# Kernel tuning notes

Measured on AMD Instinct MI355X. Metric: run time of the kernel, lower is better.

## Reference

```python
import jax, jax.numpy as jnp
import numpy as np

H = 512        # rnn_h
E = 256        # embedding_dim
ATD = 32       # action_type_emb_dim
VOCAB = 50000  # data_agent.wordcnt
NUM_ACTIONS = 10
CHECK_WEIGHT = 1.0
B, SIN, SOUT, Y = 32, 128, 32, 256
DIN = 2 * H + 1 + E + ATD + E  # dec_gru input size (y_in=True, bidir=True)


def gru_step(h, x, Wih, Whh, bih, bhh):
    # PyTorch GRUCell math
    gi = x @ Wih.T + bih
    gh = h @ Whh.T + bhh
    ir, iz, i_n = jnp.split(gi, 3, axis=-1)
    hr, hz, h_n = jnp.split(gh, 3, axis=-1)
    r = jax.nn.sigmoid(ir + hr)
    z = jax.nn.sigmoid(iz + hz)
    n = jnp.tanh(i_n + r * h_n)
    return (1.0 - z) * n + z * h


def setup_inputs() -> dict:
    key = jax.random.key(0)
    ks = iter(jax.random.split(key, 48))

    def p(shape, scale=0.05):
        return jax.random.normal(next(ks), shape, dtype=jnp.float32) * scale

    inp = {}
    inp["x"] = jax.random.randint(next(ks), (B, SIN), 0, VOCAB)
    inp["action_key"] = jax.random.randint(next(ks), (Y,), 0, VOCAB)
    inp["action_type"] = jax.random.randint(next(ks), (Y,), 0, NUM_ACTIONS + 1)
    inp["current_room"] = jax.random.randint(next(ks), (B, SOUT), 0, VOCAB)
    inp["checked"] = jax.random.uniform(next(ks), (B, SOUT + 1, Y), dtype=jnp.float32)
    inp["y"] = jax.random.uniform(next(ks), (B, SOUT, Y), dtype=jnp.float32)
    emb = p((VOCAB, E))
    inp["emb_table"] = emb.at[0].set(0.0)  # padding_idx=0
    inp["atype_table"] = p((NUM_ACTIONS + 1, ATD))
    # encoder GRU, bidirectional, 1 layer
    inp["enc_Wih_f"] = p((3 * H, E)); inp["enc_Whh_f"] = p((3 * H, H))
    inp["enc_bih_f"] = p((3 * H,));   inp["enc_bhh_f"] = p((3 * H,))
    inp["enc_Wih_b"] = p((3 * H, E)); inp["enc_Whh_b"] = p((3 * H, H))
    inp["enc_bih_b"] = p((3 * H,));   inp["enc_bhh_b"] = p((3 * H,))
    inp["trans_W"] = p((E, 2 * H)); inp["trans_b"] = p((E,))
    inp["merge_W"] = p((H, 2 * H)); inp["merge_b"] = p((H,))
    inp["dec_Wih"] = p((3 * H, DIN)); inp["dec_Whh"] = p((3 * H, H))
    inp["dec_bih"] = p((3 * H,));     inp["dec_bhh"] = p((3 * H,))
    inp["dec_W"] = p((1, H)); inp["dec_b"] = p((1,))
    inp["chk_W1"] = p((H, 2 * H + ATD + H)); inp["chk_b1"] = p((H,))
    inp["chk_W2"] = p((1, H));               inp["chk_b2"] = p((1,))
    return inp


def reference(x, action_key, action_type, current_room, checked, y,
              emb_table, atype_table,
              enc_Wih_f, enc_Whh_f, enc_bih_f, enc_bhh_f,
              enc_Wih_b, enc_Whh_b, enc_bih_b, enc_bhh_b,
              trans_W, trans_b, merge_W, merge_b,
              dec_Wih, dec_Whh, dec_bih, dec_bhh, dec_W, dec_b,
              chk_W1, chk_b1, chk_W2, chk_b2):
    emb_out = emb_table[x]  # [B, SIN, E]

    def enc_scan(Wih, Whh, bih, bhh, xs):  # xs: [S, B, E]
        def step(h, xt):
            h2 = gru_step(h, xt, Wih, Whh, bih, bhh)
            return h2, h2
        h0 = jnp.zeros((B, H), emb_out.dtype)
        return jax.lax.scan(step, h0, xs)

    xs = emb_out.transpose(1, 0, 2)
    hT_f, hs_f = enc_scan(enc_Wih_f, enc_Whh_f, enc_bih_f, enc_bhh_f, xs)
    hT_b, hs_b = enc_scan(enc_Wih_b, enc_Whh_b, enc_bih_b, enc_bhh_b, xs[::-1])
    hs_b = hs_b[::-1]
    enc_out = jnp.concatenate([hs_f, hs_b], axis=-1).transpose(1, 0, 2)  # [B, SIN, 2H]

    action_emb = emb_table[action_key]  # [Y, E]
    trans_out = jnp.tanh(enc_out @ trans_W.T + trans_b)  # [B, SIN, E]
    scores = (jnp.einsum('bse,ye->bys', emb_out, action_emb)
              + jnp.einsum('bse,ye->bys', trans_out, action_emb))
    alpha = jax.nn.softmax(scores, axis=-1)
    attention = jnp.einsum('bys,bsd->byd', alpha, enc_out)  # [B, Y, 2H]

    atype_exp = jnp.broadcast_to(atype_table[action_type], (B, Y, ATD))
    room_emb = emb_table[current_room]  # [B, SOUT, E]

    # faithful to torch: hidden [2,B,H].view(B, 2H) (layer-major flatten)
    hidden_cat = jnp.stack([hT_f, hT_b], 0).reshape(B, 2 * H)
    h0_dec = jnp.tanh(hidden_cat @ merge_W.T + merge_b)  # [B, H]
    h_dec = jnp.broadcast_to(h0_dec[:, None, :], (B, Y, H)).reshape(B * Y, H)

    y_prev = jnp.concatenate([jnp.zeros((B, 1, Y), y.dtype), y[:, :-1]], axis=1)

    att_flat = attention.reshape(B * Y, 2 * H)
    at_flat = atype_exp.reshape(B * Y, ATD)

    xs_scan = (checked[:, :SOUT].transpose(1, 0, 2),   # check_in  [T,B,Y]
               room_emb.transpose(1, 0, 2),            # room      [T,B,E]
               y_prev.transpose(1, 0, 2),              # y_{t-1}   [T,B,Y]
               y.transpose(1, 0, 2),                   # y_t       [T,B,Y]
               checked[:, 1:].transpose(1, 0, 2))      # check tgt [T,B,Y]

    def step(h, inputs):
        chk_t, room_t, yp_t, y_t, chk_next = inputs
        room_in = jnp.broadcast_to(room_t[:, None, :], (B, Y, E))
        y_in = jnp.broadcast_to((yp_t @ action_emb)[:, None, :], (B, Y, E))
        dec_in = jnp.concatenate(
            [attention, chk_t[..., None], room_in, atype_exp, y_in], axis=-1
        ).reshape(B * Y, DIN)
        h2 = gru_step(h, dec_in, dec_Wih, dec_Whh, dec_bih, dec_bhh)
        logits = (h2 @ dec_W.T + dec_b).reshape(B, Y)
        logp = jax.nn.log_softmax(logits, axis=1)
        l = -(logp * y_t).sum()
        cat = jnp.concatenate([att_flat, at_flat, h2], axis=1)
        chk = jax.nn.sigmoid(jnp.tanh(cat @ chk_W1.T + chk_b1) @ chk_W2.T + chk_b2).reshape(B, Y)
        cl = -((chk_next * jnp.log(chk) + (1.0 - chk_next) * jnp.log(1.0 - chk)) * y_t).sum() * CHECK_WEIGHT
        return h2, (l, cl)

    _, (ls, cls) = jax.lax.scan(step, h_dec, xs_scan)
    ysum = y.sum()
    loss = ls.sum() / ysum
    check_loss = cls.sum() / ysum
    return (loss + check_loss, loss, check_loss)
```

## Files before the change

kernel.cpp:

```cpp
#include <hip/hip_runtime.h>

typedef unsigned short ushort;
typedef unsigned int uint;
typedef __attribute__((ext_vector_type(8))) short short8;
typedef __attribute__((ext_vector_type(4))) float f32x4;
typedef __attribute__((ext_vector_type(4))) uint u32x4;

#define DEVI __device__ __forceinline__

#define B_ 32
#define SIN_ 128
#define SOUT_ 32
#define Y_ 256
#define H_ 512
#define E_ 256
#define TH_ 1536

DEVI float b2f(ushort u){ return __uint_as_float(((uint)u)<<16); }
DEVI ushort f2b(float f){ uint x = __float_as_uint(f); return (ushort)((x + 0x7FFFu + ((x>>16)&1u)) >> 16); }
DEVI float sigf(float x){ return 1.f/(1.f+__expf(-x)); }
DEVI float tanh_fast(float x){ return 2.f/(1.f+__expf(-2.f*x)) - 1.f; }
DEVI float splus(float x){ return fmaxf(x,0.f) + log1pf(__expf(-fabsf(x))); }
DEVI short8 cvt8(u32x4 v){ return __builtin_bit_cast(short8, v); }

DEVI uint ld_flag(const uint* p){
  uint r;
  asm volatile("global_load_dword %0, %1, off sc0 sc1\n\ts_waitcnt vmcnt(0)"
               : "=v"(r) : "v"(p) : "memory");
  return r;
}
DEVI void st_flag(uint* p, uint v){
  asm volatile("global_store_dword %0, %1, off sc0 sc1" :: "v"(p), "v"(v) : "memory");
}
DEVI void st_h16(ushort* p, uint v){
  asm volatile("global_store_short %0, %1, off sc0 sc1" :: "v"(p), "v"(v) : "memory");
}
DEVI void stf_sc1(float* p, float v){
  asm volatile("global_store_dword %0, %1, off sc0 sc1" :: "v"(p), "v"(__float_as_uint(v)) : "memory");
}
DEVI f32x4 ld4f_sc1(const float* p){
  u32x4 r;
  asm volatile("global_load_dwordx4 %0, %1, off sc0 sc1\n\ts_waitcnt vmcnt(0)"
               : "=v"(r) : "v"(p) : "memory");
  return __builtin_bit_cast(f32x4, r);
}
DEVI void ld16_sc1(const float* p, float* o){
  u32x4 r0,r1,r2,r3;
  asm volatile("global_load_dwordx4 %0, %4, off sc0 sc1\n\t"
               "global_load_dwordx4 %1, %4, off offset:16 sc0 sc1\n\t"
               "global_load_dwordx4 %2, %4, off offset:32 sc0 sc1\n\t"
               "global_load_dwordx4 %3, %4, off offset:48 sc0 sc1\n\t"
               "s_waitcnt vmcnt(0)"
               : "=&v"(r0),"=&v"(r1),"=&v"(r2),"=&v"(r3) : "v"(p) : "memory");
  *(u32x4*)(o) = r0; *(u32x4*)(o+4) = r1; *(u32x4*)(o+8) = r2; *(u32x4*)(o+12) = r3;
}
DEVI void lda2_sc1(const ushort* p0, const ushort* p1, u32x4& r0, u32x4& r1){
  asm volatile("global_load_dwordx4 %0, %2, off sc0 sc1\n\t"
               "global_load_dwordx4 %1, %3, off sc0 sc1\n\t"
               "s_waitcnt vmcnt(0)"
               : "=&v"(r0), "=&v"(r1) : "v"(p0), "v"(p1) : "memory");
}

__global__ void k_init(float* acc){ if (threadIdx.x < 4) acc[threadIdx.x] = 0.f; }

__global__ void k_wsfail(float* out){ out[0]=1.2345e8f; out[1]=2.3456e8f; out[2]=3.4567e8f; }

__global__ void k_init_enc(uint* __restrict__ flags, ushort* __restrict__ hG)
{
  const int id = blockIdx.x*256 + threadIdx.x;
  if (id < 256) flags[id] = 0u;
  if (id < 8192) ((uint4*)hG)[id] = make_uint4(0,0,0,0);
}

__global__ __launch_bounds__(256) void k_ysum(const float* __restrict__ yv, float* __restrict__ acc)
{
  __shared__ float red[256];
  float s = 0.f;
  for (long i = (long)blockIdx.x*256 + threadIdx.x; i < (long)B_*SOUT_*Y_; i += (long)gridDim.x*256) s += yv[i];
  red[threadIdx.x] = s; __syncthreads();
  for (int o=128;o;o>>=1){ if ((int)threadIdx.x<o) red[threadIdx.x] += red[threadIdx.x+o]; __syncthreads(); }
  if (threadIdx.x==0) atomicAdd(acc+2, red[0]);
}

__global__ void k_lookup(const int* __restrict__ x, const int* __restrict__ akey,
                         const int* __restrict__ atype, const int* __restrict__ croom,
                         const float* __restrict__ yv,
                         const float* __restrict__ emb, const float* __restrict__ attab,
                         ushort* __restrict__ embxs, ushort* __restrict__ aemb,
                         ushort* __restrict__ aembT, float* __restrict__ avec,
                         ushort* __restrict__ acat, ushort* __restrict__ yprev)
{
  const long N1 = (long)SIN_*B_*E_;
  const long N2 = (long)Y_*E_;
  const long N3 = (long)Y_*32;
  const long N4 = (long)SOUT_*B_*E_;
  const long N5 = (long)SOUT_*B_*Y_;
  for (long i = (long)blockIdx.x*blockDim.x + threadIdx.x; i < N1+N2+N3+N4+N5; i += (long)gridDim.x*blockDim.x){
    long id = i;
    if (id < N1){
      int e = id & 255; long sb = id >> 8; int bb = (int)(sb & 31); int s = (int)(sb >> 5);
      embxs[id] = f2b(emb[(size_t)x[bb*SIN_ + s]*E_ + e]);
    } else if ((id -= N1) < N2){
      int e = (int)(id & 255), yy = (int)(id >> 8);
      ushort v = f2b(emb[(size_t)akey[yy]*E_ + e]);
      aemb[yy*E_ + e] = v;
      aembT[e*Y_ + yy] = v;
    } else if ((id -= N2) < N3){
      int a = (int)(id & 31), yy = (int)(id >> 5);
      avec[yy*32 + a] = attab[atype[yy]*32 + a];
    } else if ((id -= N3) < N4){
      int e = (int)(id & 255); long tb = id >> 8; int bb = (int)(tb & 31); int t = (int)(tb >> 5);
      acat[(size_t)tb*512 + e] = f2b(emb[(size_t)croom[bb*SOUT_ + t]*E_ + e]);
    } else { id -= N4;
      int yy = (int)(id & 255); long tb = id >> 8; int bb = (int)(tb & 31); int t = (int)(tb >> 5);
// ... 323 lines not shown
  for (int o=1;o<64;o<<=1) m = fmaxf(m, __shfl_xor(m, o));
  const float e0 = __expf(v.x - m), e1 = __expf(v.y - m);
  float sum = e0 + e1;
  #pragma unroll
  for (int o=1;o<64;o<<=1) sum += __shfl_xor(sum, o);
  const float inv = 1.f/sum;
  ushort* a = al + (size_t)row*SIN_;
  const uint pkv = (uint)f2b(e0*inv) | ((uint)f2b(e1*inv)<<16);
  *(uint*)&a[lane*2] = pkv;
}

__global__ __launch_bounds__(512)
void k_merge(const float* __restrict__ hTf, const float* __restrict__ hTb,
             const float* __restrict__ mW, const float* __restrict__ mb,
             float* __restrict__ h0)
{
  const int b = blockIdx.x, j = threadIdx.x;
  __shared__ float hc[1024];
  for (int i=j; i<1024; i+=512){
    const int half = i >> 9, jj = i & 511;
    hc[i] = (b < 16) ? hTf[(size_t)(2*b + half)*H_ + jj] : hTb[(size_t)(2*(b-16) + half)*H_ + jj];
  }
  __syncthreads();
  float d = mb[j];
  const float* wr = mW + (size_t)j*1024;
  #pragma unroll 8
  for (int k=0;k<1024;k+=4){
    const float4 a = *(const float4*)&wr[k];
    const float4 hh = *(const float4*)&hc[k];
    d += a.x*hh.x + a.y*hh.y + a.z*hh.z + a.w*hh.w;
  }
  h0[(size_t)b*H_ + j] = tanh_fast(d);
}

__global__ void k_bcast(const float* __restrict__ h0, ushort* __restrict__ hb,
                        uint* __restrict__ flags2)
{
  for (long i = (long)blockIdx.x*blockDim.x + threadIdx.x; i < (long)8192*H_; i += (long)gridDim.x*blockDim.x){
    const int jj = (int)(i & 511); const long row = i >> 9; const int bb = (int)(row >> 8);
    hb[i] = f2b(h0[(size_t)bb*H_ + jj]);
    if (i < 256) flags2[i] = 0u;
  }
}

__global__ __launch_bounds__(512,1)
void dec_persist(ushort* __restrict__ hA, ushort* __restrict__ hB,
                 const ushort* __restrict__ Wd, const ushort* __restrict__ gib,
                 const float* __restrict__ sproj, const float* __restrict__ wchk,
                 const float* __restrict__ dbhh, const float* __restrict__ checked,
                 const float* __restrict__ decW,
                 const ushort* __restrict__ Wchk2b, const ushort* __restrict__ chkbase,
                 const float* __restrict__ cw2, const float* __restrict__ cb2v,
                 const float* __restrict__ yv,
                 float* __restrict__ LP0, float* __restrict__ LP1,
                 float* __restrict__ CP, uint* __restrict__ flags,
                 float* __restrict__ accv)
{
  __shared__ __align__(16) ushort lsA_[9216];
  __shared__ __align__(16) ushort lsB_[27648];
  __shared__ __align__(16) ushort lhold[2][9216];
  __shared__ float lred[4][128];

  const int blk = blockIdx.x;
  const int tid = threadIdx.x;
  const int bx = blk & 3, by = blk >> 2;
  const int bm = by << 7;
  const int w = tid>>6, lane = tid&63;
  const int wrh = w>>2, wc = w&3;
  const int wm = wrh<<6;
  const int l15 = lane&15, l4 = lane>>4;
  const int saRow0 = tid>>3, saK = (tid&7)<<3;
  const float cb2s = cb2v[0];
  int ep = 0;

  for (int k=0; k<=SOUT_; ++k){
    ushort* hin  = (k&1) ? hB : hA;
    ushort* hout = (k&1) ? hA : hB;
    float* LPw = (k&1) ? LP1 : LP0;
    const float* LPr = (k&1) ? LP0 : LP1;

    if (k > 0){
      const int km1 = k-1;
      if (tid < 64){
        float lossv = 0.f;
        if (tid < 32){
          const int row = blk*32 + tid;
          const int bb = row>>8, yy = row&255;
          const f32x4 cp = ld4f_sc1(&CP[(size_t)row*4]);
          const float u = cp[0]+cp[1]+cp[2]+cp[3] + cb2s;
          const float c = checked[((size_t)bb*33 + km1 + 1)*Y_ + yy];
          const float yt = yv[((size_t)bb*SOUT_ + km1)*Y_ + yy];
          lossv = yt * (c*splus(-u) + (1.f-c)*splus(u));
        }
        #pragma unroll
        for (int o=1;o<64;o<<=1) lossv += __shfl_xor(lossv, o);
        if (tid==0) atomicAdd(accv+1, lossv);
      } else if (tid < 128 && blk < 32){
        const int ln = tid - 64;
        float lf[16];
        ld16_sc1(&LPr[(size_t)blk*1024 + ln*16], lf);
        float lv[4];
        #pragma unroll
        for (int r2=0;r2<4;++r2) lv[r2] = lf[r2*4]+lf[r2*4+1]+lf[r2*4+2]+lf[r2*4+3];
        float m = fmaxf(fmaxf(lv[0],lv[1]), fmaxf(lv[2],lv[3]));
        #pragma unroll
        for (int o=1;o<64;o<<=1) m = fmaxf(m, __shfl_xor(m, o));
        float se = 0.f;
        #pragma unroll
        for (int r2=0;r2<4;++r2) se += __expf(lv[r2]-m);
        #pragma unroll
        for (int o=1;o<64;o<<=1) se += __shfl_xor(se, o);
        const float lse = m + logf(se);
        const float* yr = yv + ((size_t)blk*SOUT_ + km1)*Y_ + ln*4;
        float pl = 0.f;
        #pragma unroll
        for (int r2=0;r2<4;++r2) pl += yr[r2]*(lv[r2]-lse);
        #pragma unroll
        for (int o=1;o<64;o<<=1) pl += __shfl_xor(pl, o);
        if (ln==0) atomicAdd(accv+0, -pl);
      }
    }
    if (k == SOUT_) break;

    {
      const float* sproj_t = sproj + (size_t)k*B_*TH_;
      f32x4 acc[3][4][2];
      #pragma unroll
      for (int gg=0;gg<3;++gg)
        #pragma unroll
        for (int mi2=0;mi2<4;++mi2)
          #pragma unroll
          for (int ni2=0;ni2<2;++ni2) acc[gg][mi2][ni2] = 0.f;

      uint4 vb[6];
      #pragma unroll
      for (int i=0;i<6;++i){
        const int s = tid + (i<<9);
        const int gg = s>>10, w1 = s&1023, row = w1>>3, kc = (w1&7)<<3;
        vb[i] = *(const uint4*)&Wd[(size_t)((gg<<9) + (bx<<7) + row)*512 + kc];
      }
      const ushort* pa0 = hin + (size_t)(bm+saRow0)*512 + saK;
      const ushort* pa1 = pa0 + (size_t)64*512;
      for (int kt=0; kt<8; ++kt){
        u32x4 a0, a1;
        lda2_sc1(pa0 + kt*64, pa1 + kt*64, a0, a1);
        __syncthreads();
        *(u32x4*)&lsA_[saRow0*72 + saK] = a0;
        *(u32x4*)&lsA_[(saRow0+64)*72 + saK] = a1;
        #pragma unroll
        for (int i=0;i<6;++i){
          const int s = tid + (i<<9);
          const int gg = s>>10, w1 = s&1023, row = w1>>3, kc = (w1&7)<<3;
          *(uint4*)&lsB_[((gg<<7)+row)*72 + kc] = vb[i];
        }
        __syncthreads();
        if (kt < 7){
          const int ko = (kt+1)<<6;
          #pragma unroll
          for (int i=0;i<6;++i){
            const int s = tid + (i<<9);
            const int gg = s>>10, w1 = s&1023, row = w1>>3, kc = (w1&7)<<3;
            vb[i] = *(const uint4*)&Wd[(size_t)((gg<<9) + (bx<<7) + row)*512 + ko + kc];
          }
        }
        if ((kt>>1) == bx){
          const int half = kt&1;
          uint4* dst4 = (uint4*)&lhold[half][0];
          const uint4* src4 = (const uint4*)lsA_;
          for (int i=tid; i<1152; i+=512) dst4[i] = src4[i];
        }
        #pragma unroll
        for (int ks=0;ks<2;++ks){
          short8 af[4];
          #pragma unroll
          for (int mi2=0;mi2<4;++mi2)
            af[mi2] = *(const short8*)&lsA_[(wm + (mi2<<4) + l15)*72 + (ks<<5) + (l4<<3)];
          short8 bf[3][2];
          #pragma unroll
          for (int gg=0;gg<3;++gg)
            #pragma unroll
            for (int ni2=0;ni2<2;++ni2)
              bf[gg][ni2] = *(const short8*)&lsB_[((gg<<7) + (wc<<5) + (ni2<<4) + l15)*72 + (ks<<5) + (l4<<3)];
          #pragma unroll
          for (int gg=0;gg<3;++gg)
            #pragma unroll
            for (int mi2=0;mi2<4;++mi2)
              #pragma unroll
              for (int ni2=0;ni2<2;++ni2)
                acc[gg][mi2][ni2] = __builtin_amdgcn_mfma_f32_16x16x32_bf16(af[mi2], bf[gg][ni2], acc[gg][mi2][ni2], 0,0,0);
        }
      }
      __syncthreads();
      const int bb = by>>1;
      const float* sp = sproj_t + (size_t)bb*TH_;
      const int jbase = (bx<<7) + (wc<<5);
      float spv[3][2], wcv[3][2], bhnv[2], dwv[2];
      #pragma unroll
      for (int ni2=0;ni2<2;++ni2){
        const int j = jbase + (ni2<<4) + l15;
        spv[0][ni2] = sp[j]; spv[1][ni2] = sp[512+j]; spv[2][ni2] = sp[1024+j];
        wcv[0][ni2] = wchk[j]; wcv[1][ni2] = wchk[512+j]; wcv[2][ni2] = wchk[1024+j];
        bhnv[ni2] = dbhh[1024+j];
        dwv[ni2] = decW[j];
      }
      const float* ckrow = checked + ((size_t)(bb*33 + k))*Y_;
      const int hhalf = wc>>1, hcb = ((wc&1)<<5);
      #pragma unroll
      for (int mi2=0;mi2<4;++mi2){
        float lrow[4];
        #pragma unroll
        for (int q=0;q<4;++q) lrow[q] = 0.f;
        #pragma unroll
        for (int q=0;q<4;++q){
          const int rloc = wm + (mi2<<4) + (l4<<2) + q;
          const int row = bm + rloc;
          const float ck = ckrow[row & 255];
          #pragma unroll
          for (int ni2=0;ni2<2;++ni2){
            const int j = jbase + (ni2<<4) + l15;
            const float g0 = b2f(gib[(size_t)row*TH_ + j]);
            const float g1 = b2f(gib[(size_t)row*TH_ + 512 + j]);
            const float g2 = b2f(gib[(size_t)row*TH_ + 1024 + j]);
            const float hold = b2f(lhold[hhalf][rloc*72 + hcb + (ni2<<4) + l15]);
            const float r  = sigf(g0 + spv[0][ni2] + ck*wcv[0][ni2] + acc[0][mi2][ni2][q]);
            const float zg = sigf(g1 + spv[1][ni2] + ck*wcv[1][ni2] + acc[1][mi2][ni2][q]);
            const float n  = tanh_fast(g2 + spv[2][ni2] + ck*wcv[2][ni2] + r*(acc[2][mi2][ni2][q] + bhnv[ni2]));
            const float h2 = (1.f - zg)*n + zg*hold;
            st_h16(hout + (size_t)row*H_ + j, (uint)f2b(h2));
            lrow[q] += h2 * dwv[ni2];
          }
        }
        #pragma unroll
        for (int q=0;q<4;++q){
          float v = lrow[q];
          v += __shfl_xor(v,1); v += __shfl_xor(v,2); v += __shfl_xor(v,4); v += __shfl_xor(v,8);
          if (l15==0) lred[wc][wm + (mi2<<4) + (l4<<2) + q] = v;
        }
      }
      __syncthreads();
      if (tid < 128){
        const float s = lred[0][tid] + lred[1][tid] + lred[2][tid] + lred[3][tid];
        stf_sc1(&LPw[(size_t)(bm+tid)*4 + bx], s);
      }
    }
    ++ep;
    __syncthreads();
    if (tid == 0) st_flag(&flags[blk], (uint)ep);
    if (tid < 256){ while (ld_flag(&flags[tid]) < (uint)ep) __builtin_amdgcn_s_sleep(2); }
    __syncthreads();

    {
      const int bn = bx<<7;
      f32x4 acc2[4][2];
      #pragma unroll
      for (int mi2=0;mi2<4;++mi2)
        #pragma unroll
        for (int ni2=0;ni2<2;++ni2) acc2[mi2][ni2] = 0.f;
      uint4 vb2[2];
      #pragma unroll
      for (int i=0;i<2;++i)
        vb2[i] = *(const uint4*)&Wchk2b[(size_t)(bn+saRow0+(i<<6))*512 + saK];
      const ushort* pc0 = hout + (size_t)(bm+saRow0)*512 + saK;
      const ushort* pc1 = pc0 + (size_t)64*512;
      for (int kt=0; kt<8; ++kt){
        u32x4 a0, a1;
        lda2_sc1(pc0 + kt*64, pc1 + kt*64, a0, a1);
        __syncthreads();
        *(u32x4*)&lsA_[saRow0*72 + saK] = a0;
        *(u32x4*)&lsA_[(saRow0+64)*72 + saK] = a1;
        #pragma unroll
        for (int i=0;i<2;++i)
          *(uint4*)&lsB_[(saRow0+(i<<6))*72 + saK] = vb2[i];
        __syncthreads();
        if (kt < 7){
          const int ko = (kt+1)<<6;
          #pragma unroll
          for (int i=0;i<2;++i)
            vb2[i] = *(const uint4*)&Wchk2b[(size_t)(bn+saRow0+(i<<6))*512 + ko + saK];
        }
        #pragma unroll
        for (int ks=0;ks<2;++ks){
          short8 af[4];
          #pragma unroll
          for (int mi2=0;mi2<4;++mi2)
            af[mi2] = *(const short8*)&lsA_[(wm + (mi2<<4) + l15)*72 + (ks<<5) + (l4<<3)];
          short8 bf2[2];
          #pragma unroll
          for (int ni2=0;ni2<2;++ni2)
            bf2[ni2] = *(const short8*)&lsB_[((wc<<5) + (ni2<<4) + l15)*72 + (ks<<5) + (l4<<3)];
          #pragma unroll
          for (int mi2=0;mi2<4;++mi2)
            #pragma unroll
            for (int ni2=0;ni2<2;++ni2)
              acc2[mi2][ni2] = __builtin_amdgcn_mfma_f32_16x16x32_bf16(af[mi2], bf2[ni2], acc2[mi2][ni2], 0,0,0);
        }
      }
      float cw2v[2];
      #pragma unroll
      for (int ni2=0;ni2<2;++ni2) cw2v[ni2] = cw2[bn + (wc<<5) + (ni2<<4) + l15];
      #pragma unroll
      for (int mi2=0;mi2<4;++mi2){
        float rs2[4];
        #pragma unroll
        for (int q=0;q<4;++q) rs2[q] = 0.f;
        #pragma unroll
        for (int q=0;q<4;++q){
          const int row = bm + wm + (mi2<<4) + (l4<<2) + q;
          #pragma unroll
          for (int ni2=0;ni2<2;++ni2){
            const int col = bn + (wc<<5) + (ni2<<4) + l15;
            const float u = acc2[mi2][ni2][q] + b2f(chkbase[(size_t)row*H_ + col]);
            rs2[q] += tanh_fast(u) * cw2v[ni2];
          }
        }
        #pragma unroll
        for (int q=0;q<4;++q){
          float v = rs2[q];
          v += __shfl_xor(v,1); v += __shfl_xor(v,2); v += __shfl_xor(v,4); v += __shfl_xor(v,8);
          if (l15==0) lred[wc][wm + (mi2<<4) + (l4<<2) + q] = v;
        }
      }
      __syncthreads();
      if (tid < 128){
        const float s = lred[0][tid] + lred[1][tid] + lred[2][tid] + lred[3][tid];
        stf_sc1(&CP[(size_t)(bm+tid)*4 + bx], s);
      }
    }
    ++ep;
    __syncthreads();
    if (tid == 0) st_flag(&flags[blk], (uint)ep);
    if (tid < 256){ while (ld_flag(&flags[tid]) < (uint)ep) __builtin_amdgcn_s_sleep(2); }
    __syncthreads();
  }
}

__global__ void k_final(const float* __restrict__ acc, float* __restrict__ out)
{
  if (threadIdx.x==0){
    const float ls = acc[0], cls = acc[1], ys = acc[2];
    out[0] = (ls+cls)/ys; out[1] = ls/ys; out[2] = cls/ys;
  }
}

extern "C" void kernel_launch(void* const* d_in, const int* in_sizes, int n_in,
                              void* d_out, int out_size, void* d_ws, size_t ws_size,
                              hipStream_t stream)
{
  (void)in_sizes; (void)n_in; (void)out_size;
  const int*   x      = (const int*)d_in[0];
  const int*   akey   = (const int*)d_in[1];
  const int*   atype  = (const int*)d_in[2];
  const int*   croom  = (const int*)d_in[3];
  const float* checked= (const float*)d_in[4];
  const float* yv     = (const float*)d_in[5];
  const float* emb    = (const float*)d_in[6];
  const float* attab  = (const float*)d_in[7];
  const float* eWihF  = (const float*)d_in[8];
  const float* eWhhF  = (const float*)d_in[9];
  const float* ebihF  = (const float*)d_in[10];
  const float* ebhhF  = (const float*)d_in[11];
  const float* eWihB  = (const float*)d_in[12];
  const float* eWhhB  = (const float*)d_in[13];
  const float* ebihB  = (const float*)d_in[14];
  const float* ebhhB  = (const float*)d_in[15];
  const float* transW = (const float*)d_in[16];
  const float* transb = (const float*)d_in[17];
  const float* mergeW = (const float*)d_in[18];
  const float* mergeb = (const float*)d_in[19];
  const float* dWih   = (const float*)d_in[20];
  const float* dWhh   = (const float*)d_in[21];
  const float* dbih   = (const float*)d_in[22];
  const float* dbhh   = (const float*)d_in[23];
  const float* dW     = (const float*)d_in[24];
  const float* cW1    = (const float*)d_in[26];
  const float* cb1    = (const float*)d_in[27];
  const float* cW2    = (const float*)d_in[28];
  const float* cb2    = (const float*)d_in[29];

  char* base = (char*)d_ws;
  size_t off = 0;
  auto alloc = [&](size_t bytes)->char*{ char* p = base + off; off += (bytes + 255) & ~(size_t)255; return p; };

  float*  accv   = (float*)alloc(256);
  ushort* embxs  = (ushort*)alloc((size_t)SIN_*B_*E_*2);
  ushort* aemb   = (ushort*)alloc((size_t)Y_*E_*2);
  ushort* aembT  = (ushort*)alloc((size_t)Y_*E_*2);
  float*  avec   = (float*)alloc((size_t)Y_*32*4);
  ushort* yprev  = (ushort*)alloc((size_t)SOUT_*B_*Y_*2);
  ushort* acat   = (ushort*)alloc((size_t)SOUT_*B_*512*2);
  ushort* gi_fb  = (ushort*)alloc((size_t)2*SIN_*B_*TH_*2);
  ushort* gi_f   = gi_fb;
  ushort* gi_b   = gi_fb + (size_t)SIN_*B_*TH_;
  ushort* gibase = gi_fb;
  ushort* encout = (ushort*)alloc((size_t)B_*SIN_*1024*2);
  ushort* encoutT= (ushort*)alloc((size_t)B_*1024*SIN_*2);
  float*  hTf    = (float*)alloc((size_t)B_*H_*4);
  float*  hTb    = (float*)alloc((size_t)B_*H_*4);
  float*  h0dec  = (float*)alloc((size_t)B_*H_*4);
  ushort* esum   = (ushort*)alloc((size_t)B_*SIN_*E_*2);
  float*  scores = (float*)alloc((size_t)B_*Y_*SIN_*4);
  ushort* alpha  = (ushort*)alloc((size_t)B_*Y_*SIN_*2);
  ushort* att    = (ushort*)alloc((size_t)8192*1024*2);
  ushort* chkbase= (ushort*)alloc((size_t)8192*H_*2);
  float*  addy   = (float*)alloc((size_t)Y_*TH_*4);
  float*  addcy  = (float*)alloc((size_t)Y_*H_*4);
  float*  sproj  = (float*)alloc((size_t)SOUT_*B_*TH_*4);
  float*  wchk   = (float*)alloc((size_t)TH_*4);
  float*  dbhhrz = (float*)alloc((size_t)TH_*4);
  ushort* WihFb  = (ushort*)alloc((size_t)TH_*E_*2);
  ushort* WihBb  = (ushort*)alloc((size_t)TH_*E_*2);
  ushort* Wtrb   = (ushort*)alloc((size_t)E_*1024*2);
  ushort* Wattb  = (ushort*)alloc((size_t)TH_*1024*2);
  ushort* Wcat2b = (ushort*)alloc((size_t)TH_*512*2);
  ushort* W1attb = (ushort*)alloc((size_t)H_*1024*2);
  ushort* Wdecb  = (ushort*)alloc((size_t)TH_*512*2);
  ushort* Wchk2b = (ushort*)alloc((size_t)512*512*2);
  ushort* h2bA   = (ushort*)alloc((size_t)8192*H_*2);
  ushort* h2bB   = (ushort*)alloc((size_t)8192*H_*2);
  float*  CP     = (float*)alloc((size_t)8192*4*4);
  float*  LP0    = (float*)alloc((size_t)8192*4*4);
  float*  LP1    = (float*)alloc((size_t)8192*4*4);
  ushort* hG     = (ushort*)alloc((size_t)2*2*32*512*2);
  uint*   flags  = (uint*)alloc((size_t)256*4);
  uint*   flags2 = (uint*)alloc((size_t)256*4);

  if (off > ws_size){ k_wsfail<<<1,1,0,stream>>>((float*)d_out); return; }

  float* outp = (float*)d_out;

  k_init<<<dim3(1), dim3(64), 0, stream>>>(accv);
  k_init_enc<<<dim3(64), dim3(256), 0, stream>>>(flags, hG);
  k_ysum<<<dim3(256), dim3(256), 0, stream>>>(yv, accv);
  k_lookup<<<dim3(2048), dim3(256), 0, stream>>>(x, akey, atype, croom, yv, emb, attab,
                                                 embxs, aemb, aembT, avec, acat, yprev);
  k_convall<<<dim3(2048), dim3(256), 0, stream>>>(eWihF, eWihB, transW, dWih, cW1, dWhh,
                                                  WihFb, WihBb, Wtrb, Wattb, Wcat2b, W1attb, Wdecb, Wchk2b);
  k_prep2<<<dim3(1024), dim3(256), 0, stream>>>(avec, dWih, dbih, cW1, cb1, dbhh,
                                                addy, addcy, wchk, dbhhrz);

  gemm_nt<(GF_BIAS|GF_WBF16)><<<dim3(12,32,1), dim3(256), 0, stream>>>(
    embxs, WihFb, ebihF, nullptr, 0, nullptr, gi_f, TH_, E_, E_, E_, 0, 0L,0L,0L, nullptr);
  gemm_nt<(GF_BIAS|GF_WBF16)><<<dim3(12,32,1), dim3(256), 0, stream>>>(
    embxs, WihBb, ebihB, nullptr, 0, nullptr, gi_b, TH_, E_, E_, E_, 0, 0L,0L,0L, nullptr);

  enc_persist<<<dim3(64), dim3(256), 0, stream>>>(eWhhF, eWhhB, ebhhF, ebhhB, gi_f, gi_b,
                                                  hG, flags, encout, encoutT, hTf, hTb);

  gemm_nt<(GF_BIAS|GF_TANH|GF_ESUM|GF_WBF16)><<<dim3(2,32,1), dim3(256), 0, stream>>>(
    encout, Wtrb, transb, nullptr, 0, nullptr, esum, E_, 1024, 1024, 1024, 0, 0L,0L,0L, embxs);

  gemm_nt<GF_WF32><<<dim3(1,2,32), dim3(256), 0, stream>>>(
    aemb, esum, nullptr, nullptr, 0, scores, nullptr, SIN_, E_, E_, E_, 0,
    0L, (long)SIN_*E_, (long)Y_*SIN_, nullptr);
  k_softmax<<<dim3(2048), dim3(256), 0, stream>>>(scores, alpha);

  gemm_nt<GF_WBF16><<<dim3(8,2,32), dim3(256), 0, stream>>>(
    alpha, encoutT, nullptr, nullptr, 0, nullptr, att, 1024, SIN_, SIN_, SIN_, 0,
    (long)Y_*SIN_, (long)1024*SIN_, (long)Y_*1024, nullptr);

  k_merge<<<dim3(32), dim3(512), 0, stream>>>(hTf, hTb, mergeW, mergeb, h0dec);

  gemm_nt<GF_WBF16><<<dim3(2,8,1), dim3(256), 0, stream>>>(
    yprev, aembT, nullptr, nullptr, 0, nullptr, acat+256, 512, Y_, Y_, Y_, 0, 0L,0L,0L, nullptr);
  gemm_nt<(GF_BIAS|GF_WF32)><<<dim3(12,8,1), dim3(256), 0, stream>>>(
    acat, Wcat2b, dbhhrz, nullptr, 0, sproj, nullptr, TH_, 512, 512, 512, 0, 0L,0L,0L, nullptr);

  gemm_nt<(GF_WBF16|GF_ADDY)><<<dim3(12,64,1), dim3(256), 0, stream>>>(
    att, Wattb, nullptr, addy, TH_, nullptr, gibase, TH_, 1024, 1024, 1024, 0, 0L,0L,0L, nullptr);
  gemm_nt<(GF_WBF16|GF_ADDY)><<<dim3(4,64,1), dim3(256), 0, stream>>>(
    att, W1attb, nullptr, addcy, H_, nullptr, chkbase, H_, 1024, 1024, 1024, 0, 0L,0L,0L, nullptr);

  k_bcast<<<dim3(1024), dim3(256), 0, stream>>>(h0dec, h2bA, flags2);

  dec_persist<<<dim3(256), dim3(512), 0, stream>>>(
    h2bA, h2bB, Wdecb, gibase, sproj, wchk, dbhh, checked, dW,
    Wchk2b, chkbase, cW2, cb2, yv, LP0, LP1, CP, flags2, accv);

  k_final<<<dim3(1), dim3(1), 0, stream>>>(accv, outp);
}
```

Measured before the change: 3.916 ms.

## Fuse check GEMM into next decoder step and drop one grid barrier per step

```diff
diff --git a/kernel.cpp b/kernel.cpp
--- a/kernel.cpp
+++ b/kernel.cpp
@@ -54,12 +54,12 @@
                : "=&v"(r0),"=&v"(r1),"=&v"(r2),"=&v"(r3) : "v"(p) : "memory");
   *(u32x4*)(o) = r0; *(u32x4*)(o+4) = r1; *(u32x4*)(o+8) = r2; *(u32x4*)(o+12) = r3;
 }
-DEVI void lda2_sc1(const ushort* p0, const ushort* p1, u32x4& r0, u32x4& r1){
+DEVI void lda2_issue(const ushort* p0, const ushort* p1, u32x4& r0, u32x4& r1){
   asm volatile("global_load_dwordx4 %0, %2, off sc0 sc1\n\t"
-               "global_load_dwordx4 %1, %3, off sc0 sc1\n\t"
-               "s_waitcnt vmcnt(0)"
+               "global_load_dwordx4 %1, %3, off sc0 sc1"
                : "=&v"(r0), "=&v"(r1) : "v"(p0), "v"(p1) : "memory");
 }
+DEVI void wait_vm0(){ asm volatile("s_waitcnt vmcnt(0)" ::: "memory"); }
 
 __global__ void k_init(float* acc){ if (threadIdx.x < 4) acc[threadIdx.x] = 0.f; }
 
@@ -489,12 +489,13 @@
                  const ushort* __restrict__ Wchk2b, const ushort* __restrict__ chkbase,
                  const float* __restrict__ cw2, const float* __restrict__ cb2v,
                  const float* __restrict__ yv,
-                 float* __restrict__ LP0, float* __restrict__ LP1,
-                 float* __restrict__ CP, uint* __restrict__ flags,
-                 float* __restrict__ accv)
+                 float* __restrict__ LP0, float* __restrict__ LP1, float* __restrict__ LP2,
+                 float* __restrict__ CP0, float* __restrict__ CP1,
+                 uint* __restrict__ flags, float* __restrict__ accv)
 {
   __shared__ __align__(16) ushort lsA_[9216];
   __shared__ __align__(16) ushort lsB_[27648];
+  __shared__ __align__(16) ushort lsB2_[9216];
   __shared__ __align__(16) ushort lhold[2][9216];
   __shared__ float lred[4][128];
 
@@ -511,22 +512,31 @@
   int ep = 0;
 
   for (int k=0; k<=SOUT_; ++k){
-    ushort* hin  = (k&1) ? hB : hA;
+    const ushort* hin = (k&1) ? hB : hA;
     ushort* hout = (k&1) ? hA : hB;
-    float* LPw = (k&1) ? LP1 : LP0;
-    const float* LPr = (k&1) ? LP0 : LP1;
-
-    if (k > 0){
-      const int km1 = k-1;
+    const int km3 = k % 3;
+    float* LPw = (km3==0) ? LP0 : ((km3==1) ? LP1 : LP2);
+    float* CPw = ((k-1)&1) ? CP1 : CP0;
+
+    const ushort* pa0 = hin + (size_t)(bm+saRow0)*512 + saK;
+    const ushort* pa1 = pa0 + (size_t)64*512;
+    u32x4 raA0, raB0, raA1, raB1;
+    lda2_issue(pa0, pa1, raA0, raB0);
+
+    if (k >= 2){
+      const int lt = k-2;
+      const int lm3 = lt % 3;
+      const float* LPr = (lm3==0) ? LP0 : ((lm3==1) ? LP1 : LP2);
+      const float* CPr = (lt&1) ? CP1 : CP0;
       if (tid < 64){
         float lossv = 0.f;
         if (tid < 32){
           const int row = blk*32 + tid;
           const int bb = row>>8, yy = row&255;
-          const f32x4 cp = ld4f_sc1(&CP[(size_t)row*4]);
+          const f32x4 cp = ld4f_sc1(&CPr[(size_t)row*4]);
           const float u = cp[0]+cp[1]+cp[2]+cp[3] + cb2s;
-          const float c = checked[((size_t)bb*33 + km1 + 1)*Y_ + yy];
-          const float yt = yv[((size_t)bb*SOUT_ + km1)*Y_ + yy];
+          const float c = checked[((size_t)bb*33 + lt + 1)*Y_ + yy];
+          const float yt = yv[((size_t)bb*SOUT_ + lt)*Y_ + yy];
           lossv = yt * (c*splus(-u) + (1.f-c)*splus(u));
         }
         #pragma unroll
@@ -548,7 +558,7 @@
         #pragma unroll
         for (int o=1;o<64;o<<=1) se += __shfl_xor(se, o);
         const float lse = m + logf(se);
-        const float* yr = yv + ((size_t)blk*SOUT_ + km1)*Y_ + ln*4;
+        const float* yr = yv + ((size_t)blk*SOUT_ + lt)*Y_ + ln*4;
         float pl = 0.f;
         #pragma unroll
         for (int r2=0;r2<4;++r2) pl += yr[r2]*(lv[r2]-lse);
@@ -557,42 +567,66 @@
         if (ln==0) atomicAdd(accv+0, -pl);
       }
     }
-    if (k == SOUT_) break;
-
-    {
-      const float* sproj_t = sproj + (size_t)k*B_*TH_;
-      f32x4 acc[3][4][2];
-      #pragma unroll
-      for (int gg=0;gg<3;++gg)
-        #pragma unroll
-        for (int mi2=0;mi2<4;++mi2)
-          #pragma unroll
-          for (int ni2=0;ni2<2;++ni2) acc[gg][mi2][ni2] = 0.f;
-
-      uint4 vb[6];
+
+    uint4 vb[6];
+    if (k < SOUT_){
       #pragma unroll
       for (int i=0;i<6;++i){
         const int s = tid + (i<<9);
         const int gg = s>>10, w1 = s&1023, row = w1>>3, kc = (w1&7)<<3;
         vb[i] = *(const uint4*)&Wd[(size_t)((gg<<9) + (bx<<7) + row)*512 + kc];
       }
-      const ushort* pa0 = hin + (size_t)(bm+saRow0)*512 + saK;
-      const ushort* pa1 = pa0 + (size_t)64*512;
-      for (int kt=0; kt<8; ++kt){
-        u32x4 a0, a1;
-        lda2_sc1(pa0 + kt*64, pa1 + kt*64, a0, a1);
-        __syncthreads();
-        *(u32x4*)&lsA_[saRow0*72 + saK] = a0;
-        *(u32x4*)&lsA_[(saRow0+64)*72 + saK] = a1;
+    }
+    uint4 vb2[2];
+    if (k >= 1){
+      #pragma unroll
+      for (int i=0;i<2;++i)
+        vb2[i] = *(const uint4*)&Wchk2b[(size_t)((bx<<7)+saRow0+(i<<6))*512 + saK];
+    }
+
+    f32x4 acc[3][4][2];
+    #pragma unroll
+    for (int gg=0;gg<3;++gg)
+      #pragma unroll
+      for (int mi2=0;mi2<4;++mi2)
+        #pragma unroll
+        for (int ni2=0;ni2<2;++ni2) acc[gg][mi2][ni2] = 0.f;
+    f32x4 acc2[4][2];
+    #pragma unroll
+    for (int mi2=0;mi2<4;++mi2)
+      #pragma unroll
+      for (int ni2=0;ni2<2;++ni2) acc2[mi2][ni2] = 0.f;
+
+    #pragma unroll
+    for (int kt=0; kt<8; ++kt){
+      wait_vm0();
+      __syncthreads();
+      if (kt&1){
+        *(u32x4*)&lsA_[saRow0*72 + saK] = raA1;
+        *(u32x4*)&lsA_[(saRow0+64)*72 + saK] = raB1;
+      } else {
+        *(u32x4*)&lsA_[saRow0*72 + saK] = raA0;
+        *(u32x4*)&lsA_[(saRow0+64)*72 + saK] = raB0;
+      }
+      if (k < SOUT_){
         #pragma unroll
         for (int i=0;i<6;++i){
           const int s = tid + (i<<9);
           const int gg = s>>10, w1 = s&1023, row = w1>>3, kc = (w1&7)<<3;
           *(uint4*)&lsB_[((gg<<7)+row)*72 + kc] = vb[i];
         }
-        __syncthreads();
-        if (kt < 7){
-          const int ko = (kt+1)<<6;
+      }
+      if (k >= 1){
+        #pragma unroll
+        for (int i=0;i<2;++i)
+          *(uint4*)&lsB2_[(saRow0+(i<<6))*72 + saK] = vb2[i];
+      }
+      __syncthreads();
+      if (kt < 7){
+        const int ko = (kt+1)<<6;
+        if (kt&1) lda2_issue(pa0 + ko, pa1 + ko, raA0, raB0);
+        else      lda2_issue(pa0 + ko, pa1 + ko, raA1, raB1);
+        if (k < SOUT_){
           #pragma unroll
           for (int i=0;i<6;++i){
             const int s = tid + (i<<9);
@@ -600,18 +634,25 @@
             vb[i] = *(const uint4*)&Wd[(size_t)((gg<<9) + (bx<<7) + row)*512 + ko + kc];
           }
         }
-        if ((kt>>1) == bx){
-          const int half = kt&1;
-          uint4* dst4 = (uint4*)&lhold[half][0];
-          const uint4* src4 = (const uint4*)lsA_;
-          for (int i=tid; i<1152; i+=512) dst4[i] = src4[i];
+        if (k >= 1){
+          #pragma unroll
+          for (int i=0;i<2;++i)
+            vb2[i] = *(const uint4*)&Wchk2b[(size_t)((bx<<7)+saRow0+(i<<6))*512 + ko + saK];
         }
-        #pragma unroll
-        for (int ks=0;ks<2;++ks){
-          short8 af[4];
-          #pragma unroll
-          for (int mi2=0;mi2<4;++mi2)
-            af[mi2] = *(const short8*)&lsA_[(wm + (mi2<<4) + l15)*72 + (ks<<5) + (l4<<3)];
+      }
+      if (k < SOUT_ && (kt>>1) == bx){
+        const int half = kt&1;
+        uint4* dst4 = (uint4*)&lhold[half][0];
+        const uint4* src4 = (const uint4*)lsA_;
+        for (int i=tid; i<1152; i+=512) dst4[i] = src4[i];
+      }
+      #pragma unroll
+      for (int ks=0;ks<2;++ks){
+        short8 af[4];
+        #pragma unroll
+        for (int mi2=0;mi2<4;++mi2)
+          af[mi2] = *(const short8*)&lsA_[(wm + (mi2<<4) + l15)*72 + (ks<<5) + (l4<<3)];
+        if (k < SOUT_){
           short8 bf[3][2];
           #pragma unroll
           for (int gg=0;gg<3;++gg)
@@ -626,10 +667,23 @@
               for (int ni2=0;ni2<2;++ni2)
                 acc[gg][mi2][ni2] = __builtin_amdgcn_mfma_f32_16x16x32_bf16(af[mi2], bf[gg][ni2], acc[gg][mi2][ni2], 0,0,0);
         }
-      }
-      __syncthreads();
-      const int bb = by>>1;
-      const float* sp = sproj_t + (size_t)bb*TH_;
+        if (k >= 1){
+          short8 bf2[2];
+          #pragma unroll
+          for (int ni2=0;ni2<2;++ni2)
+            bf2[ni2] = *(const short8*)&lsB2_[((wc<<5) + (ni2<<4) + l15)*72 + (ks<<5) + (l4<<3)];
+          #pragma unroll
+          for (int mi2=0;mi2<4;++mi2)
+            #pragma unroll
+            for (int ni2=0;ni2<2;++ni2)
+              acc2[mi2][ni2] = __builtin_amdgcn_mfma_f32_16x16x32_bf16(af[mi2], bf2[ni2], acc2[mi2][ni2], 0,0,0);
+        }
+      }
+    }
+    __syncthreads();
+
+    if (k < SOUT_){
+      const float* sp = sproj + (size_t)k*B_*TH_ + (size_t)(by>>1)*TH_;
       const int jbase = (bx<<7) + (wc<<5);
       float spv[3][2], wcv[3][2], bhnv[2], dwv[2];
       #pragma unroll
@@ -640,7 +694,7 @@
         bhnv[ni2] = dbhh[1024+j];
         dwv[ni2] = decW[j];
       }
-      const float* ckrow = checked + ((size_t)(bb*33 + k))*Y_;
+      const float* ckrow = checked + ((size_t)((by>>1)*33 + k))*Y_;
       const int hhalf = wc>>1, hcb = ((wc&1)<<5);
       #pragma unroll
       for (int mi2=0;mi2<4;++mi2){
@@ -680,58 +734,10 @@
         stf_sc1(&LPw[(size_t)(bm+tid)*4 + bx], s);
       }
     }
-    ++ep;
     __syncthreads();
-    if (tid == 0) st_flag(&flags[blk], (uint)ep);
-    if (tid < 256){ while (ld_flag(&flags[tid]) < (uint)ep) __builtin_amdgcn_s_sleep(2); }
-    __syncthreads();
-
-    {
+
+    if (k >= 1){
       const int bn = bx<<7;
-      f32x4 acc2[4][2];
-      #pragma unroll
-      for (int mi2=0;mi2<4;++mi2)
-        #pragma unroll
-        for (int ni2=0;ni2<2;++ni2) acc2[mi2][ni2] = 0.f;
-      uint4 vb2[2];
-      #pragma unroll
-      for (int i=0;i<2;++i)
-        vb2[i] = *(const uint4*)&Wchk2b[(size_t)(bn+saRow0+(i<<6))*512 + saK];
-      const ushort* pc0 = hout + (size_t)(bm+saRow0)*512 + saK;
-      const ushort* pc1 = pc0 + (size_t)64*512;
-      for (int kt=0; kt<8; ++kt){
-        u32x4 a0, a1;
-        lda2_sc1(pc0 + kt*64, pc1 + kt*64, a0, a1);
-        __syncthreads();
-        *(u32x4*)&lsA_[saRow0*72 + saK] = a0;
-        *(u32x4*)&lsA_[(saRow0+64)*72 + saK] = a1;
-        #pragma unroll
-        for (int i=0;i<2;++i)
-          *(uint4*)&lsB_[(saRow0+(i<<6))*72 + saK] = vb2[i];
-        __syncthreads();
-        if (kt < 7){
-          const int ko = (kt+1)<<6;
-          #pragma unroll
-          for (int i=0;i<2;++i)
-            vb2[i] = *(const uint4*)&Wchk2b[(size_t)(bn+saRow0+(i<<6))*512 + ko + saK];
-        }
-        #pragma unroll
-        for (int ks=0;ks<2;++ks){
-          short8 af[4];
-          #pragma unroll
-          for (int mi2=0;mi2<4;++mi2)
-            af[mi2] = *(const short8*)&lsA_[(wm + (mi2<<4) + l15)*72 + (ks<<5) + (l4<<3)];
-          short8 bf2[2];
-          #pragma unroll
-          for (int ni2=0;ni2<2;++ni2)
-            bf2[ni2] = *(const short8*)&lsB_[((wc<<5) + (ni2<<4) + l15)*72 + (ks<<5) + (l4<<3)];
-          #pragma unroll
-          for (int mi2=0;mi2<4;++mi2)
-            #pragma unroll
-            for (int ni2=0;ni2<2;++ni2)
-              acc2[mi2][ni2] = __builtin_amdgcn_mfma_f32_16x16x32_bf16(af[mi2], bf2[ni2], acc2[mi2][ni2], 0,0,0);
-        }
-      }
       float cw2v[2];
       #pragma unroll
       for (int ni2=0;ni2<2;++ni2) cw2v[ni2] = cw2[bn + (wc<<5) + (ni2<<4) + l15];
@@ -760,14 +766,60 @@
       __syncthreads();
       if (tid < 128){
         const float s = lred[0][tid] + lred[1][tid] + lred[2][tid] + lred[3][tid];
-        stf_sc1(&CP[(size_t)(bm+tid)*4 + bx], s);
-      }
-    }
+        stf_sc1(&CPw[(size_t)(bm+tid)*4 + bx], s);
+      }
+    }
+
     ++ep;
     __syncthreads();
     if (tid == 0) st_flag(&flags[blk], (uint)ep);
     if (tid < 256){ while (ld_flag(&flags[tid]) < (uint)ep) __builtin_amdgcn_s_sleep(2); }
     __syncthreads();
+  }
+
+  {
+    const int lt = SOUT_-1;
+    const int lm3 = lt % 3;
+    const float* LPr = (lm3==0) ? LP0 : ((lm3==1) ? LP1 : LP2);
+    const float* CPr = (lt&1) ? CP1 : CP0;
+    if (tid < 64){
+      float lossv = 0.f;
+      if (tid < 32){
+        const int row = blk*32 + tid;
+        const int bb = row>>8, yy = row&255;
+        const f32x4 cp = ld4f_sc1(&CPr[(size_t)row*4]);
+        const float u = cp[0]+cp[1]+cp[2]+cp[3] + cb2s;
+        const float c = checked[((size_t)bb*33 + lt + 1)*Y_ + yy];
+        const float yt = yv[((size_t)bb*SOUT_ + lt)*Y_ + yy];
+        lossv = yt * (c*splus(-u) + (1.f-c)*splus(u));
+      }
+      #pragma unroll
+      for (int o=1;o<64;o<<=1) lossv += __shfl_xor(lossv, o);
+      if (tid==0) atomicAdd(accv+1, lossv);
+    } else if (tid < 128 && blk < 32){
+      const int ln = tid - 64;
+      float lf[16];
+      ld16_sc1(&LPr[(size_t)blk*1024 + ln*16], lf);
+      float lv[4];
+      #pragma unroll
+      for (int r2=0;r2<4;++r2) lv[r2] = lf[r2*4]+lf[r2*4+1]+lf[r2*4+2]+lf[r2*4+3];
+      float m = fmaxf(fmaxf(lv[0],lv[1]), fmaxf(lv[2],lv[3]));
+      #pragma unroll
+      for (int o=1;o<64;o<<=1) m = fmaxf(m, __shfl_xor(m, o));
+      float se = 0.f;
+      #pragma unroll
+      for (int r2=0;r2<4;++r2) se += __expf(lv[r2]-m);
+      #pragma unroll
+      for (int o=1;o<64;o<<=1) se += __shfl_xor(se, o);
+      const float lse = m + logf(se);
+      const float* yr = yv + ((size_t)blk*SOUT_ + lt)*Y_ + ln*4;
+      float pl = 0.f;
+      #pragma unroll
+      for (int r2=0;r2<4;++r2) pl += yr[r2]*(lv[r2]-lse);
+      #pragma unroll
+      for (int o=1;o<64;o<<=1) pl += __shfl_xor(pl, o);
+      if (ln==0) atomicAdd(accv+0, -pl);
+    }
   }
 }
 
@@ -854,9 +906,11 @@
   ushort* Wchk2b = (ushort*)alloc((size_t)512*512*2);
   ushort* h2bA   = (ushort*)alloc((size_t)8192*H_*2);
   ushort* h2bB   = (ushort*)alloc((size_t)8192*H_*2);
-  float*  CP     = (float*)alloc((size_t)8192*4*4);
+  float*  CP0    = (float*)alloc((size_t)8192*4*4);
+  float*  CP1    = (float*)alloc((size_t)8192*4*4);
   float*  LP0    = (float*)alloc((size_t)8192*4*4);
   float*  LP1    = (float*)alloc((size_t)8192*4*4);
+  float*  LP2    = (float*)alloc((size_t)8192*4*4);
   ushort* hG     = (ushort*)alloc((size_t)2*2*32*512*2);
   uint*   flags  = (uint*)alloc((size_t)256*4);
   uint*   flags2 = (uint*)alloc((size_t)256*4);
@@ -911,7 +965,7 @@
 
   dec_persist<<<dim3(256), dim3(512), 0, stream>>>(
     h2bA, h2bB, Wdecb, gibase, sproj, wchk, dbhh, checked, dW,
-    Wchk2b, chkbase, cW2, cb2, yv, LP0, LP1, CP, flags2, accv);
+    Wchk2b, chkbase, cW2, cb2, yv, LP0, LP1, LP2, CP0, CP1, flags2, accv);
 
   k_final<<<dim3(1), dim3(1), 0, stream>>>(accv, outp);
 }
```

New measurement: 4.338 ms. 1.11x slower.

## Prefetch hidden-state tiles ahead and coalesce h writes through LDS

Applied to the files above, without the earlier changes.

```diff
diff --git a/kernel.cpp b/kernel.cpp
--- a/kernel.cpp
+++ b/kernel.cpp
@@ -37,6 +37,9 @@
 }
 DEVI void stf_sc1(float* p, float v){
   asm volatile("global_store_dword %0, %1, off sc0 sc1" :: "v"(p), "v"(__float_as_uint(v)) : "memory");
+}
+DEVI void st16_sc1(ushort* p, u32x4 v){
+  asm volatile("global_store_dwordx4 %0, %1, off sc0 sc1" :: "v"(p), "v"(v) : "memory");
 }
 DEVI f32x4 ld4f_sc1(const float* p){
   u32x4 r;
@@ -54,12 +57,15 @@
                : "=&v"(r0),"=&v"(r1),"=&v"(r2),"=&v"(r3) : "v"(p) : "memory");
   *(u32x4*)(o) = r0; *(u32x4*)(o+4) = r1; *(u32x4*)(o+8) = r2; *(u32x4*)(o+12) = r3;
 }
-DEVI void lda2_sc1(const ushort* p0, const ushort* p1, u32x4& r0, u32x4& r1){
-  asm volatile("global_load_dwordx4 %0, %2, off sc0 sc1\n\t"
-               "global_load_dwordx4 %1, %3, off sc0 sc1\n\t"
-               "s_waitcnt vmcnt(0)"
-               : "=&v"(r0), "=&v"(r1) : "v"(p0), "v"(p1) : "memory");
-}
+DEVI void lda4(const ushort* p0, const ushort* p1, u32x4* r){
+  asm volatile("global_load_dwordx4 %0, %4, off sc0 sc1\n\t"
+               "global_load_dwordx4 %1, %5, off sc0 sc1\n\t"
+               "global_load_dwordx4 %2, %4, off offset:128 sc0 sc1\n\t"
+               "global_load_dwordx4 %3, %5, off offset:128 sc0 sc1"
+               : "=&v"(r[0]),"=&v"(r[1]),"=&v"(r[2]),"=&v"(r[3])
+               : "v"(p0), "v"(p1) : "memory");
+}
+DEVI void wait_vm0(){ asm volatile("s_waitcnt vmcnt(0)" ::: "memory"); }
 
 __global__ void k_init(float* acc){ if (threadIdx.x < 4) acc[threadIdx.x] = 0.f; }
 
@@ -578,58 +584,72 @@
       }
       const ushort* pa0 = hin + (size_t)(bm+saRow0)*512 + saK;
       const ushort* pa1 = pa0 + (size_t)64*512;
-      for (int kt=0; kt<8; ++kt){
-        u32x4 a0, a1;
-        lda2_sc1(pa0 + kt*64, pa1 + kt*64, a0, a1);
-        __syncthreads();
-        *(u32x4*)&lsA_[saRow0*72 + saK] = a0;
-        *(u32x4*)&lsA_[(saRow0+64)*72 + saK] = a1;
-        #pragma unroll
-        for (int i=0;i<6;++i){
-          const int s = tid + (i<<9);
-          const int gg = s>>10, w1 = s&1023, row = w1>>3, kc = (w1&7)<<3;
-          *(uint4*)&lsB_[((gg<<7)+row)*72 + kc] = vb[i];
-        }
-        __syncthreads();
-        if (kt < 7){
-          const int ko = (kt+1)<<6;
+      u32x4 ra[4], rb[4];
+      lda4(pa0, pa1, ra);
+      wait_vm0();
+      lda4(pa0+128, pa1+128, rb);
+      #pragma unroll
+      for (int g=0; g<4; ++g){
+        #pragma unroll
+        for (int j2=0; j2<2; ++j2){
+          const int kt = g*2 + j2;
+          const u32x4 x0 = (g&1) ? rb[2*j2]   : ra[2*j2];
+          const u32x4 x1 = (g&1) ? rb[2*j2+1] : ra[2*j2+1];
+          __syncthreads();
+          *(u32x4*)&lsA_[saRow0*72 + saK] = x0;
+          *(u32x4*)&lsA_[(saRow0+64)*72 + saK] = x1;
           #pragma unroll
           for (int i=0;i<6;++i){
             const int s = tid + (i<<9);
             const int gg = s>>10, w1 = s&1023, row = w1>>3, kc = (w1&7)<<3;
-            vb[i] = *(const uint4*)&Wd[(size_t)((gg<<9) + (bx<<7) + row)*512 + ko + kc];
+            *(uint4*)&lsB_[((gg<<7)+row)*72 + kc] = vb[i];
+          }
+          __syncthreads();
+          if (kt < 7){
+            const int ko = (kt+1)<<6;
+            #pragma unroll
+            for (int i=0;i<6;++i){
+              const int s = tid + (i<<9);
+              const int gg = s>>10, w1 = s&1023, row = w1>>3, kc = (w1&7)<<3;
+              vb[i] = *(const uint4*)&Wd[(size_t)((gg<<9) + (bx<<7) + row)*512 + ko + kc];
+            }
+          }
+          if ((kt>>1) == bx){
+            const int half = kt&1;
+            uint4* dst4 = (uint4*)&lhold[half][0];
+            const uint4* src4 = (const uint4*)lsA_;
+            for (int i2=tid; i2<1152; i2+=512) dst4[i2] = src4[i2];
+          }
+          #pragma unroll
+          for (int ks=0;ks<2;++ks){
+            short8 af[4];
+            #pragma unroll
+            for (int mi2=0;mi2<4;++mi2)
+              af[mi2] = *(const short8*)&lsA_[(wm + (mi2<<4) + l15)*72 + (ks<<5) + (l4<<3)];
+            short8 bf[3][2];
+            #pragma unroll
+            for (int gg=0;gg<3;++gg)
+              #pragma unroll
+              for (int ni2=0;ni2<2;++ni2)
+                bf[gg][ni2] = *(const short8*)&lsB_[((gg<<7) + (wc<<5) + (ni2<<4) + l15)*72 + (ks<<5) + (l4<<3)];
+            #pragma unroll
+            for (int gg=0;gg<3;++gg)
+              #pragma unroll
+              for (int mi2=0;mi2<4;++mi2)
+                #pragma unroll
+                for (int ni2=0;ni2<2;++ni2)
+                  acc[gg][mi2][ni2] = __builtin_amdgcn_mfma_f32_16x16x32_bf16(af[mi2], bf[gg][ni2], acc[gg][mi2][ni2], 0,0,0);
           }
         }
-        if ((kt>>1) == bx){
-          const int half = kt&1;
-          uint4* dst4 = (uint4*)&lhold[half][0];
-          const uint4* src4 = (const uint4*)lsA_;
-          for (int i=tid; i<1152; i+=512) dst4[i] = src4[i];
+        if (g < 3) wait_vm0();
+        if (g < 2){
+          const ushort* q0 = pa0 + (size_t)(g+2)*128;
+          const ushort* q1 = pa1 + (size_t)(g+2)*128;
+          if (g&1) lda4(q0, q1, rb); else lda4(q0, q1, ra);
         }
-        #pragma unroll
-        for (int ks=0;ks<2;++ks){
-          short8 af[4];
-          #pragma unroll
-          for (int mi2=0;mi2<4;++mi2)
-            af[mi2] = *(const short8*)&lsA_[(wm + (mi2<<4) + l15)*72 + (ks<<5) + (l4<<3)];
-          short8 bf[3][2];
-          #pragma unroll
-          for (int gg=0;gg<3;++gg)
-            #pragma unroll
-            for (int ni2=0;ni2<2;++ni2)
-              bf[gg][ni2] = *(const short8*)&lsB_[((gg<<7) + (wc<<5) + (ni2<<4) + l15)*72 + (ks<<5) + (l4<<3)];
-          #pragma unroll
-          for (int gg=0;gg<3;++gg)
-            #pragma unroll
-            for (int mi2=0;mi2<4;++mi2)
-              #pragma unroll
-              for (int ni2=0;ni2<2;++ni2)
-                acc[gg][mi2][ni2] = __builtin_amdgcn_mfma_f32_16x16x32_bf16(af[mi2], bf[gg][ni2], acc[gg][mi2][ni2], 0,0,0);
-        }
       }
       __syncthreads();
-      const int bb = by>>1;
-      const float* sp = sproj_t + (size_t)bb*TH_;
+      const float* sp = sproj_t + (size_t)(by>>1)*TH_;
       const int jbase = (bx<<7) + (wc<<5);
       float spv[3][2], wcv[3][2], bhnv[2], dwv[2];
       #pragma unroll
@@ -640,7 +660,7 @@
         bhnv[ni2] = dbhh[1024+j];
         dwv[ni2] = decW[j];
       }
-      const float* ckrow = checked + ((size_t)(bb*33 + k))*Y_;
+      const float* ckrow = checked + ((size_t)((by>>1)*33 + k))*Y_;
       const int hhalf = wc>>1, hcb = ((wc&1)<<5);
       #pragma unroll
       for (int mi2=0;mi2<4;++mi2){
@@ -663,7 +683,7 @@
             const float zg = sigf(g1 + spv[1][ni2] + ck*wcv[1][ni2] + acc[1][mi2][ni2][q]);
             const float n  = tanh_fast(g2 + spv[2][ni2] + ck*wcv[2][ni2] + r*(acc[2][mi2][ni2][q] + bhnv[ni2]));
             const float h2 = (1.f - zg)*n + zg*hold;
-            st_h16(hout + (size_t)row*H_ + j, (uint)f2b(h2));
+            lsB_[rloc*128 + (wc<<5) + (ni2<<4) + l15] = f2b(h2);
             lrow[q] += h2 * dwv[ni2];
           }
         }
@@ -679,6 +699,13 @@
         const float s = lred[0][tid] + lred[1][tid] + lred[2][tid] + lred[3][tid];
         stf_sc1(&LPw[(size_t)(bm+tid)*4 + bx], s);
       }
+      #pragma unroll
+      for (int i=0;i<4;++i){
+        const int idx = tid + (i<<9);
+        const int r2 = idx>>4, c8 = (idx&15)<<3;
+        const u32x4 v = *(const u32x4*)&lsB_[r2*128 + c8];
+        st16_sc1(hout + (size_t)(bm+r2)*512 + (bx<<7) + c8, v);
+      }
     }
     ++ep;
     __syncthreads();
@@ -699,37 +726,52 @@
         vb2[i] = *(const uint4*)&Wchk2b[(size_t)(bn+saRow0+(i<<6))*512 + saK];
       const ushort* pc0 = hout + (size_t)(bm+saRow0)*512 + saK;
       const ushort* pc1 = pc0 + (size_t)64*512;
-      for (int kt=0; kt<8; ++kt){
-        u32x4 a0, a1;
-        lda2_sc1(pc0 + kt*64, pc1 + kt*64, a0, a1);
-        __syncthreads();
-        *(u32x4*)&lsA_[saRow0*72 + saK] = a0;
-        *(u32x4*)&lsA_[(saRow0+64)*72 + saK] = a1;
-        #pragma unroll
-        for (int i=0;i<2;++i)
-          *(uint4*)&lsB_[(saRow0+(i<<6))*72 + saK] = vb2[i];
-        __syncthreads();
-        if (kt < 7){
-          const int ko = (kt+1)<<6;
+      u32x4 ra[4], rb[4];
+      lda4(pc0, pc1, ra);
+      wait_vm0();
+      lda4(pc0+128, pc1+128, rb);
+      #pragma unroll
+      for (int g=0; g<4; ++g){
+        #pragma unroll
+        for (int j2=0; j2<2; ++j2){
+          const int kt = g*2 + j2;
+          const u32x4 x0 = (g&1) ? rb[2*j2]   : ra[2*j2];
+          const u32x4 x1 = (g&1) ? rb[2*j2+1] : ra[2*j2+1];
+          __syncthreads();
+          *(u32x4*)&lsA_[saRow0*72 + saK] = x0;
+          *(u32x4*)&lsA_[(saRow0+64)*72 + saK] = x1;
           #pragma unroll
           for (int i=0;i<2;++i)
-            vb2[i] = *(const uint4*)&Wchk2b[(size_t)(bn+saRow0+(i<<6))*512 + ko + saK];
-        }
-        #pragma unroll
-        for (int ks=0;ks<2;++ks){
-          short8 af[4];
+            *(uint4*)&lsB_[(saRow0+(i<<6))*72 + saK] = vb2[i];
+          __syncthreads();
+          if (kt < 7){
+            const int ko = (kt+1)<<6;
+            #pragma unroll
+            for (int i=0;i<2;++i)
+              vb2[i] = *(const uint4*)&Wchk2b[(size_t)(bn+saRow0+(i<<6))*512 + ko + saK];
+          }
           #pragma unroll
-          for (int mi2=0;mi2<4;++mi2)
-            af[mi2] = *(const short8*)&lsA_[(wm + (mi2<<4) + l15)*72 + (ks<<5) + (l4<<3)];
-          short8 bf2[2];
-          #pragma unroll
-          for (int ni2=0;ni2<2;++ni2)
-            bf2[ni2] = *(const short8*)&lsB_[((wc<<5) + (ni2<<4) + l15)*72 + (ks<<5) + (l4<<3)];
-          #pragma unroll
-          for (int mi2=0;mi2<4;++mi2)
+          for (int ks=0;ks<2;++ks){
+            short8 af[4];
+            #pragma unroll
+            for (int mi2=0;mi2<4;++mi2)
+              af[mi2] = *(const short8*)&lsA_[(wm + (mi2<<4) + l15)*72 + (ks<<5) + (l4<<3)];
+            short8 bf2[2];
             #pragma unroll
             for (int ni2=0;ni2<2;++ni2)
-              acc2[mi2][ni2] = __builtin_amdgcn_mfma_f32_16x16x32_bf16(af[mi2], bf2[ni2], acc2[mi2][ni2], 0,0,0);
+              bf2[ni2] = *(const short8*)&lsB_[((wc<<5) + (ni2<<4) + l15)*72 + (ks<<5) + (l4<<3)];
+            #pragma unroll
+            for (int mi2=0;mi2<4;++mi2)
+              #pragma unroll
+              for (int ni2=0;ni2<2;++ni2)
+                acc2[mi2][ni2] = __builtin_amdgcn_mfma_f32_16x16x32_bf16(af[mi2], bf2[ni2], acc2[mi2][ni2], 0,0,0);
+          }
+        }
+        if (g < 3) wait_vm0();
+        if (g < 2){
+          const ushort* q0 = pc0 + (size_t)(g+2)*128;
+          const ushort* q1 = pc1 + (size_t)(g+2)*128;
+          if (g&1) lda4(q0, q1, rb); else lda4(q0, q1, ra);
         }
       }
       float cw2v[2];
```

Result: slower. 5.136 ms (+31.1%).
